# Kernel tuning notes

Hardware: AMD Instinct MI355X
Metric: run time of the kernel (lower is better)

Reference implementation:

```python
import jax, jax.numpy as jnp
import numpy as np

B_, L_, H_, P_ = 8, 4096, 512, 256
DT_LO, DT_HI = 1e-3, 4e-3  # keep Heinsen log-space weights in fp32 range for L=4096


def setup_inputs() -> dict:
    key = jax.random.key(0)
    ks = jax.random.split(key, 8)
    u = jax.random.normal(ks[0], (B_, L_, H_), dtype=jnp.float32)
    # Diagonal continuous-time state matrix Lambda (HiPPO-N-like: Re=-0.5, structured imag parts)
    lambda_re = -0.5 * jnp.ones((P_,), dtype=jnp.float32)
    lambda_im = jnp.pi * (jnp.arange(P_, dtype=jnp.float32) + 1.0)
    # Input/output projections (complex, stored as re/im pairs)
    B_re = jax.random.normal(ks[1], (P_, H_), dtype=jnp.float32) / jnp.sqrt(float(H_))
    B_im = jax.random.normal(ks[2], (P_, H_), dtype=jnp.float32) / jnp.sqrt(float(H_))
    C_re = jax.random.normal(ks[3], (H_, P_), dtype=jnp.float32) / jnp.sqrt(float(P_))
    C_im = jax.random.normal(ks[4], (H_, P_), dtype=jnp.float32) / jnp.sqrt(float(P_))
    D = jax.random.normal(ks[5], (H_,), dtype=jnp.float32)
    # Per-state learnable log-timescales, log-uniform in [DT_LO, DT_HI]
    log_delta = jax.random.uniform(ks[6], (P_,), dtype=jnp.float32,
                                   minval=jnp.log(DT_LO), maxval=jnp.log(DT_HI))
    return {"u": u, "lambda_re": lambda_re, "lambda_im": lambda_im,
            "B_re": B_re, "B_im": B_im, "C_re": C_re, "C_im": C_im,
            "D": D, "log_delta": log_delta}


def reference(u, lambda_re, lambda_im, B_re, B_im, C_re, C_im, D, log_delta):
    # --- ZOH discretization (eq. 6 of S5 paper) ---
    lam = lambda_re + 1j * lambda_im                     # (P,) complex64
    delta = jnp.exp(log_delta)                           # (P,)
    lambda_bar = jnp.exp(lam * delta)                    # (P,) complex
    B_tilde = B_re + 1j * B_im                           # (P,H)
    B_bar = ((lambda_bar - 1.0) / lam)[:, None] * B_tilde  # (P,H)

    # --- input projection: Bu_k = B_bar @ u_k ---
    Bu = jnp.einsum('blh,ph->blp', u.astype(B_bar.dtype), B_bar)  # (B,L,P) complex

    # --- Heinsen log-space parallel scan: x_k = lambda_bar * x_{k-1} + Bu_k ---
    L = u.shape[1]
    log_lambda = jnp.log(lambda_bar)                     # (P,) complex
    k = jnp.arange(L, dtype=jnp.float32)
    weights = jnp.exp(k[:, None] * log_lambda[None, :])  # (L,P) complex
    xs = weights[None] * jnp.cumsum(Bu / weights[None], axis=1)  # (B,L,P)

    # --- output: y_k = 2*Re(C_tilde x_k) + D*u_k (conjugate symmetry) ---
    C_tilde = C_re + 1j * C_im                           # (H,P)
    y = 2.0 * jnp.real(jnp.einsum('blp,hp->blh', xs, C_tilde)) + D * u
    return y
```

## Files before the change

kernel.cpp:

```cpp
#include <hip/hip_runtime.h>
#include <hip/hip_bf16.h>
#include <math.h>

#define HH 512
#define PP 256
#define LSEQ 4096
#define BB 8
#define MTOT (BB*LSEQ)
#define N2P 512

typedef __attribute__((ext_vector_type(8))) short bf16x8;
typedef __attribute__((ext_vector_type(4))) float f32x4;
typedef __attribute__((ext_vector_type(8))) unsigned short u16x8;
typedef __attribute__((ext_vector_type(4))) unsigned short u16x4;

#define SWZ(row) (((((row) & 7) ^ (((row) >> 3) & 7)) << 4))

__device__ inline unsigned short f2b(float x) {
    return __builtin_bit_cast(unsigned short, __float2bfloat16(x));
}
__device__ inline float b2f(unsigned short h) {
    union { unsigned int u; float f; } v; v.u = ((unsigned int)h) << 16;
    return v.f;
}

#define GLOAD16(gp, lp) __builtin_amdgcn_global_load_lds( \
    (const __attribute__((address_space(1))) unsigned int*)(gp), \
    (__attribute__((address_space(3))) unsigned int*)(lp), 16, 0, 0)

__device__ inline size_t panel_off(int r, int k) {
    int nblk = r >> 7, rl = r & 127;
    int kblk = k >> 6, kl = k & 63;
    int c = kl >> 3, j = kl & 7;
    return (size_t)(nblk * 8 + kblk) * 16384 + rl * 128 + ((c * 16) ^ SWZ(rl)) + j * 2;
}

__global__ void prep_w1_k(const float* __restrict__ lre, const float* __restrict__ lim,
                          const float* __restrict__ logd,
                          const float* __restrict__ Bre, const float* __restrict__ Bim,
                          char* __restrict__ W1s, float2* __restrict__ lamb) {
    int idx = blockIdx.x * 256 + threadIdx.x;
    if (idx >= PP * HH) return;
    int p = idx >> 9;
    int h = idx & (HH - 1);
    float delta = expf(logd[p]);
    float lr = lre[p], li = lim[p];
    float er = expf(lr * delta);
    float th = li * delta;
    float lbr = er * cosf(th), lbi = er * sinf(th);
    if (h == 0) lamb[p] = make_float2(lbr, lbi);
    float a = lbr - 1.0f, b = lbi;
    float n2 = lr * lr + li * li;
    float gr = (a * lr + b * li) / n2;
    float gi = (b * lr - a * li) / n2;
    float br = Bre[idx], bi = Bim[idx];
    *(unsigned short*)(W1s + panel_off(p, h))      = f2b(gr * br - gi * bi);
    *(unsigned short*)(W1s + panel_off(PP + p, h)) = f2b(gr * bi + gi * br);
}

__global__ void prep_w2_k(const float* __restrict__ Cre, const float* __restrict__ Cim,
                          char* __restrict__ W2s) {
    int idx = blockIdx.x * 256 + threadIdx.x;
    if (idx >= HH * N2P) return;
    int h = idx >> 9;
    int k = idx & 511;
    float v = (k < PP) ? 2.0f * Cre[(size_t)h * PP + k]
                       : -2.0f * Cim[(size_t)h * PP + (k - PP)];
    *(unsigned short*)(W2s + panel_off(h, k)) = f2b(v);
}

#define TILE_COMPUTE(ABUF, BBUF) { \
    bf16x8 af[4][2], bfv[2][2]; \
    _Pragma("unroll") for (int f = 0; f < 4; ++f) { \
      int ar = wm + f * 16 + (lane & 15); \
      _Pragma("unroll") for (int kk = 0; kk < 2; ++kk) \
        af[f][kk] = *(const bf16x8*)((ABUF) + ar * 128 + ((kk * 64 + (lane >> 4) * 16) ^ SWZ(ar))); } \
    _Pragma("unroll") for (int g = 0; g < 2; ++g) { \
      int br = wn + g * 16 + (lane & 15); \
      _Pragma("unroll") for (int kk = 0; kk < 2; ++kk) \
        bfv[g][kk] = *(const bf16x8*)((BBUF) + br * 128 + ((kk * 64 + (lane >> 4) * 16) ^ SWZ(br))); } \
    _Pragma("unroll") for (int f = 0; f < 4; ++f) \
      _Pragma("unroll") for (int g = 0; g < 2; ++g) \
        _Pragma("unroll") for (int kk = 0; kk < 2; ++kk) \
          acc[f][g] = __builtin_amdgcn_mfma_f32_16x16x32_bf16(af[f][kk], bfv[g][kk], acc[f][g], 0, 0, 0); }

__global__ __launch_bounds__(512, 4) void gemm1_k(const float* __restrict__ u,
                                                  const char* __restrict__ W1s,
                                                  unsigned short* __restrict__ T1) {
    __shared__ char smem[65536];
    const int tid = threadIdx.x, wave = tid >> 6, lane = tid & 63;
    const int swz = (blockIdx.x & 7) * 128 + (blockIdx.x >> 3);
    const int m0 = (swz >> 2) * 128;
    const int nblk = swz & 3, n0 = nblk * 128;
    const int wm = (wave >> 2) * 64, wn = (wave & 3) * 32;
    const int arow = tid >> 2, acol = tid & 3;

    float4 av[4];
    f32x4 acc[4][2] = {};

#define G1_A_LOAD(K0) { \
    const float* src = &u[(size_t)(m0 + arow) * HH + (K0) + acol * 16]; \
    av[0] = *(const float4*)src;       av[1] = *(const float4*)(src + 4); \
    av[2] = *(const float4*)(src + 8); av[3] = *(const float4*)(src + 12); }

#define G1_A_WRITE(ABUF) { \
    bf16x8 p0, p1; \
    p0[0] = (short)f2b(av[0].x); p0[1] = (short)f2b(av[0].y); \
    p0[2] = (short)f2b(av[0].z); p0[3] = (short)f2b(av[0].w); \
    p0[4] = (short)f2b(av[1].x); p0[5] = (short)f2b(av[1].y); \
    p0[6] = (short)f2b(av[1].z); p0[7] = (short)f2b(av[1].w); \
    p1[0] = (short)f2b(av[2].x); p1[1] = (short)f2b(av[2].y); \
    p1[2] = (short)f2b(av[2].z); p1[3] = (short)f2b(av[2].w); \
    p1[4] = (short)f2b(av[3].x); p1[5] = (short)f2b(av[3].y); \
    p1[6] = (short)f2b(av[3].z); p1[7] = (short)f2b(av[3].w); \
    *(bf16x8*)((ABUF) + arow * 128 + ((acol * 32)      ^ SWZ(arow))) = p0; \
    *(bf16x8*)((ABUF) + arow * 128 + ((acol * 32 + 16) ^ SWZ(arow))) = p1; }

#define G1_B_GLOAD(K0, BBUF) { \
    const char* pan = W1s + (size_t)(nblk * 8 + ((K0) >> 6)) * 16384 + tid * 16; \
    GLOAD16(pan, (BBUF) + tid * 16); \
    GLOAD16(pan + 8192, (BBUF) + tid * 16 + 8192); }

    char* A0 = smem;          char* B0 = smem + 16384;
    char* A1 = smem + 32768;  char* B1 = smem + 49152;

    G1_B_GLOAD(0, B0); G1_A_LOAD(0); G1_A_WRITE(A0);
    asm volatile("s_waitcnt vmcnt(0)" ::: "memory");
    __syncthreads();

    for (int t = 0; t < 8; ++t) {
        char* Ac = (t & 1) ? A1 : A0; char* Bc = (t & 1) ? B1 : B0;
        char* An = (t & 1) ? A0 : A1; char* Bn = (t & 1) ? B0 : B1;
        if (t < 7) { G1_B_GLOAD((t + 1) * 64, Bn); G1_A_LOAD((t + 1) * 64); }
        TILE_COMPUTE(Ac, Bc);
        if (t < 7) { G1_A_WRITE(An); }
        asm volatile("s_waitcnt vmcnt(0)" ::: "memory");
        __syncthreads();
    }

    {
        char* ep = smem;
        #pragma unroll
        for (int f = 0; f < 4; ++f) {
            #pragma unroll
            for (int g = 0; g < 2; ++g) {
                int r = wn + g * 16 + (lane & 15);
                int mb = (wm + f * 16 + ((lane >> 4) << 2)) * 2;
                u16x4 pk;
                pk[0] = f2b(acc[f][g][0]); pk[1] = f2b(acc[f][g][1]);
                pk[2] = f2b(acc[f][g][2]); pk[3] = f2b(acc[f][g][3]);
                *(u16x4*)(ep + r * 256 + (mb ^ ((r & 7) << 4))) = pk;
            }
        }
        __syncthreads();
        #pragma unroll
        for (int it = 0; it < 4; ++it) {
            int r = it * 32 + (tid >> 4);
            int mc = tid & 15;
            u16x8 v = *(const u16x8*)(ep + r * 256 + ((mc * 16) ^ ((r & 7) << 4)));
            *(u16x8*)&T1[(size_t)(n0 + r) * MTOT + m0 + mc * 8] = v;
        }
    }
}

__global__ __launch_bounds__(512, 4) void gemm2_k(const unsigned short* __restrict__ Xs,
                                                  const char* __restrict__ W2s,
                                                  float* __restrict__ y,
                                                  const float* __restrict__ u,
                                                  const float* __restrict__ D) {
    __shared__ char smem[65536];
    const int tid = threadIdx.x, wave = tid >> 6, lane = tid & 63;
    const int swz = (blockIdx.x & 7) * 128 + (blockIdx.x >> 3);
    const int m0 = (swz >> 2) * 128;
    const int nblk = swz & 3, n0 = nblk * 128;
    const int wm = (wave >> 2) * 64, wn = (wave & 3) * 32;
    const int kr = tid >> 5;
    const int mc4 = tid & 31;

    u16x4 xv[4];
    f32x4 acc[4][2] = {};

#define G2_A_LOAD(K0) { \
    _Pragma("unroll") for (int kk = 0; kk < 4; ++kk) \
        xv[kk] = *(const u16x4*)&Xs[(size_t)((K0) + kr * 4 + kk) * MTOT + m0 + mc4 * 4]; }

#define G2_A_WRITE(ABUF) { \
    _Pragma("unroll") for (int j = 0; j < 4; ++j) { \
        int m = mc4 * 4 + j; \
        u16x4 o; o[0] = xv[0][j]; o[1] = xv[1][j]; o[2] = xv[2][j]; o[3] = xv[3][j]; \
        *(u16x4*)((ABUF) + m * 128 + ((kr * 8) ^ SWZ(m))) = o; } }

#define G2_B_GLOAD(K0, BBUF) { \
    const char* pan = W2s + (size_t)(nblk * 8 + ((K0) >> 6)) * 16384 + tid * 16; \
    GLOAD16(pan, (BBUF) + tid * 16); \
    GLOAD16(pan + 8192, (BBUF) + tid * 16 + 8192); }

    char* A0 = smem;          char* B0 = smem + 16384;
    char* A1 = smem + 32768;  char* B1 = smem + 49152;

    G2_B_GLOAD(0, B0); G2_A_LOAD(0); G2_A_WRITE(A0);
    asm volatile("s_waitcnt vmcnt(0)" ::: "memory");
    __syncthreads();

    for (int t = 0; t < 8; ++t) {
        char* Ac = (t & 1) ? A1 : A0; char* Bc = (t & 1) ? B1 : B0;
        char* An = (t & 1) ? A0 : A1; char* Bn = (t & 1) ? B0 : B1;
        if (t < 7) { G2_B_GLOAD((t + 1) * 64, Bn); G2_A_LOAD((t + 1) * 64); }
        TILE_COMPUTE(Ac, Bc);
        if (t < 7) { G2_A_WRITE(An); }
        asm volatile("s_waitcnt vmcnt(0)" ::: "memory");
        __syncthreads();
    }

    float* epi = (float*)smem;
    float* myepi = epi + wave * 2048;
    #pragma unroll
    for (int f = 0; f < 4; ++f) {
        #pragma unroll
        for (int g = 0; g < 2; ++g) {
            int ml = f * 16 + ((lane >> 4) << 2);
            int hl = g * 16 + (lane & 15);
            #pragma unroll
            for (int i = 0; i < 4; ++i)
                myepi[(ml + i) * 32 + hl] = acc[f][g][i];
        }
    }
    __syncthreads();

    #pragma unroll
    for (int it = 0; it < 8; ++it) {
        int idx = it * 512 + tid;
        int ml = idx >> 5, c = idx & 31;
        int w = ((ml >> 6) << 2) + (c >> 3);
        const float4 v = *(const float4*)(epi + w * 2048 + (ml & 63) * 32 + (c & 7) * 4);
        int grow = m0 + ml, gcol = n0 + c * 4;
        const float4 uv = *(const float4*)&u[(size_t)grow * HH + gcol];
        const float4 dv = *(const float4*)&D[gcol];
        float4 o = make_float4(v.x + dv.x * uv.x, v.y + dv.y * uv.y,
                               v.z + dv.z * uv.z, v.w + dv.w * uv.w);
        *(float4*)&y[(size_t)grow * HH + gcol] = o;
    }
}

__global__ __launch_bounds__(256) void scan_k(const unsigned short* __restrict__ T1,
                                              unsigned short* __restrict__ Xs,
                                              const float2* __restrict__ lamb) {
    const int b = blockIdx.x >> 8;
    const int p = blockIdx.x & 255;
    const int t = threadIdx.x;
    const float2 L = lamb[p];

    const size_t baseRe = (size_t)p * MTOT + (size_t)b * LSEQ + t * 16;
    const size_t baseIm = (size_t)(PP + p) * MTOT + (size_t)b * LSEQ + t * 16;

    u16x8 r0 = *(const u16x8*)&T1[baseRe];
    u16x8 r1 = *(const u16x8*)&T1[baseRe + 8];
    u16x8 i0 = *(const u16x8*)&T1[baseIm];
    u16x8 i1 = *(const u16x8*)&T1[baseIm + 8];

    float re[16], im[16];
    #pragma unroll
    for (int j = 0; j < 8; ++j) {
        re[j] = b2f(r0[j]); re[8 + j] = b2f(r1[j]);
        im[j] = b2f(i0[j]); im[8 + j] = b2f(i1[j]);
    }

    float sr = 0.f, si = 0.f;
    #pragma unroll
    for (int j = 0; j < 16; ++j) {
        float nsr = L.x * sr - L.y * si + re[j];
        si = L.x * si + L.y * sr + im[j];
        sr = nsr;
    }

    __shared__ float cr[256], ci[256];
    cr[t] = sr; ci[t] = si;
    __syncthreads();

    float wr = L.x, wi = L.y;
    #pragma unroll
    for (int q = 0; q < 4; ++q) { float nr = wr * wr - wi * wi; wi = 2.f * wr * wi; wr = nr; }

    for (int off = 1; off < 256; off <<= 1) {
        float pr = 0.f, pi = 0.f;
        const bool has = (t >= off);
        if (has) { pr = cr[t - off]; pi = ci[t - off]; }
        __syncthreads();
        if (has) {
            sr += wr * pr - wi * pi;
            si += wr * pi + wi * pr;
            cr[t] = sr; ci[t] = si;
        }
        __syncthreads();
        float nr = wr * wr - wi * wi; wi = 2.f * wr * wi; wr = nr;
    }

    float xr = 0.f, xi = 0.f;
    if (t > 0) { xr = cr[t - 1]; xi = ci[t - 1]; }

    u16x8 o0, o1, o2, o3;
    #pragma unroll
    for (int j = 0; j < 16; ++j) {
        float nr = L.x * xr - L.y * xi + re[j];
        xi = L.x * xi + L.y * xr + im[j];
        xr = nr;
        if (j < 8) { o0[j] = f2b(xr); o2[j] = f2b(xi); }
        else       { o1[j - 8] = f2b(xr); o3[j - 8] = f2b(xi); }
    }
    *(u16x8*)&Xs[baseRe]     = o0;
    *(u16x8*)&Xs[baseRe + 8] = o1;
    *(u16x8*)&Xs[baseIm]     = o2;
    *(u16x8*)&Xs[baseIm + 8] = o3;
}


extern "C" void kernel_launch(void* const* d_in, const int* in_sizes, int n_in,
                              void* d_out, int out_size, void* d_ws, size_t ws_size,
                              hipStream_t stream) {
    const float* u    = (const float*)d_in[0];
    const float* lre  = (const float*)d_in[1];
    const float* lim  = (const float*)d_in[2];
    const float* Bre  = (const float*)d_in[3];
    const float* Bim  = (const float*)d_in[4];
    const float* Cre  = (const float*)d_in[5];
    const float* Cim  = (const float*)d_in[6];
    const float* Dv   = (const float*)d_in[7];
    const float* logd = (const float*)d_in[8];
    float* out = (float*)d_out;

    char* ws = (char*)d_ws;
    char*           W1s  = ws;
    char*           W2s  = ws + (512 << 10);
    float2*         lamb = (float2*)(ws + (1 << 20));
    unsigned short* Xs   = (unsigned short*)(ws + (1 << 20) + 4096);

    unsigned short* T1 = (unsigned short*)d_out;

    prep_w1_k<<<(PP * HH) / 256, 256, 0, stream>>>(lre, lim, logd, Bre, Bim, W1s, lamb);
    prep_w2_k<<<(HH * N2P) / 256, 256, 0, stream>>>(Cre, Cim, W2s);

    gemm1_k<<<1024, 512, 0, stream>>>(u, W1s, T1);
    scan_k<<<BB * PP, 256, 0, stream>>>(T1, Xs, lamb);
    gemm2_k<<<1024, 512, 0, stream>>>(Xs, W2s, out, u, Dv);
}
```

Measured before the change: 99.74 us.

## Prefetch A operand two K-tiles ahead with register double-buffering in both GEMMs

Both GEMM kernels now keep two register sets for the A-operand global loads and issue each load two iterations ahead. The per-iteration wait drops from a full vmcnt(0) to vmcnt(4), so loads for the following tile can stay in flight across the barrier. The goal is to hide global-load latency on the u and Xs streams behind MFMA compute. In exchange it uses more VGPRs, which may limit occupancy under the 512-thread launch bounds, and correctness now depends on hand-counted vmcnt values matching the order in which loads are issued.

```diff
diff --git a/kernel.cpp b/kernel.cpp
--- a/kernel.cpp
+++ b/kernel.cpp
@@ -95,24 +95,24 @@
     const int wm = (wave >> 2) * 64, wn = (wave & 3) * 32;
     const int arow = tid >> 2, acol = tid & 3;
 
-    float4 av[4];
+    float4 av0[4], av1[4];
     f32x4 acc[4][2] = {};
 
-#define G1_A_LOAD(K0) { \
+#define G1_A_LOAD(SET, K0) { \
     const float* src = &u[(size_t)(m0 + arow) * HH + (K0) + acol * 16]; \
-    av[0] = *(const float4*)src;       av[1] = *(const float4*)(src + 4); \
-    av[2] = *(const float4*)(src + 8); av[3] = *(const float4*)(src + 12); }
-
-#define G1_A_WRITE(ABUF) { \
+    SET[0] = *(const float4*)src;       SET[1] = *(const float4*)(src + 4); \
+    SET[2] = *(const float4*)(src + 8); SET[3] = *(const float4*)(src + 12); }
+
+#define G1_A_WRITE(SET, ABUF) { \
     bf16x8 p0, p1; \
-    p0[0] = (short)f2b(av[0].x); p0[1] = (short)f2b(av[0].y); \
-    p0[2] = (short)f2b(av[0].z); p0[3] = (short)f2b(av[0].w); \
-    p0[4] = (short)f2b(av[1].x); p0[5] = (short)f2b(av[1].y); \
-    p0[6] = (short)f2b(av[1].z); p0[7] = (short)f2b(av[1].w); \
-    p1[0] = (short)f2b(av[2].x); p1[1] = (short)f2b(av[2].y); \
-    p1[2] = (short)f2b(av[2].z); p1[3] = (short)f2b(av[2].w); \
-    p1[4] = (short)f2b(av[3].x); p1[5] = (short)f2b(av[3].y); \
-    p1[6] = (short)f2b(av[3].z); p1[7] = (short)f2b(av[3].w); \
+    p0[0] = (short)f2b(SET[0].x); p0[1] = (short)f2b(SET[0].y); \
+    p0[2] = (short)f2b(SET[0].z); p0[3] = (short)f2b(SET[0].w); \
+    p0[4] = (short)f2b(SET[1].x); p0[5] = (short)f2b(SET[1].y); \
+    p0[6] = (short)f2b(SET[1].z); p0[7] = (short)f2b(SET[1].w); \
+    p1[0] = (short)f2b(SET[2].x); p1[1] = (short)f2b(SET[2].y); \
+    p1[2] = (short)f2b(SET[2].z); p1[3] = (short)f2b(SET[2].w); \
+    p1[4] = (short)f2b(SET[3].x); p1[5] = (short)f2b(SET[3].y); \
+    p1[6] = (short)f2b(SET[3].z); p1[7] = (short)f2b(SET[3].w); \
     *(bf16x8*)((ABUF) + arow * 128 + ((acol * 32)      ^ SWZ(arow))) = p0; \
     *(bf16x8*)((ABUF) + arow * 128 + ((acol * 32 + 16) ^ SWZ(arow))) = p1; }
 
@@ -124,17 +124,29 @@
     char* A0 = smem;          char* B0 = smem + 16384;
     char* A1 = smem + 32768;  char* B1 = smem + 49152;
 
-    G1_B_GLOAD(0, B0); G1_A_LOAD(0); G1_A_WRITE(A0);
-    asm volatile("s_waitcnt vmcnt(0)" ::: "memory");
+    G1_A_LOAD(av1, 0);
+    G1_B_GLOAD(0, B0);
+    G1_A_LOAD(av0, 64);
+    asm volatile("s_waitcnt vmcnt(4)" ::: "memory");
+    G1_A_WRITE(av1, A0);
     __syncthreads();
 
+    #pragma unroll
     for (int t = 0; t < 8; ++t) {
         char* Ac = (t & 1) ? A1 : A0; char* Bc = (t & 1) ? B1 : B0;
         char* An = (t & 1) ? A0 : A1; char* Bn = (t & 1) ? B0 : B1;
-        if (t < 7) { G1_B_GLOAD((t + 1) * 64, Bn); G1_A_LOAD((t + 1) * 64); }
+        if (t < 7) G1_B_GLOAD((t + 1) * 64, Bn);
+        if (t < 6) {
+            if ((t & 1) == 0) { G1_A_LOAD(av1, (t + 2) * 64); }
+            else              { G1_A_LOAD(av0, (t + 2) * 64); }
+        }
         TILE_COMPUTE(Ac, Bc);
-        if (t < 7) { G1_A_WRITE(An); }
-        asm volatile("s_waitcnt vmcnt(0)" ::: "memory");
+        if (t < 7) {
+            if ((t & 1) == 0) { G1_A_WRITE(av0, An); }
+            else              { G1_A_WRITE(av1, An); }
+        }
+        if (t < 6)       { asm volatile("s_waitcnt vmcnt(4)" ::: "memory"); }
+        else if (t == 6) { asm volatile("s_waitcnt vmcnt(0)" ::: "memory"); }
         __syncthreads();
     }
 
@@ -177,17 +189,17 @@
     const int kr = tid >> 5;
     const int mc4 = tid & 31;
 
-    u16x4 xv[4];
+    u16x4 xv0[4], xv1[4];
     f32x4 acc[4][2] = {};
 
-#define G2_A_LOAD(K0) { \
+#define G2_A_LOAD(SET, K0) { \
     _Pragma("unroll") for (int kk = 0; kk < 4; ++kk) \
-        xv[kk] = *(const u16x4*)&Xs[(size_t)((K0) + kr * 4 + kk) * MTOT + m0 + mc4 * 4]; }
-
-#define G2_A_WRITE(ABUF) { \
+        SET[kk] = *(const u16x4*)&Xs[(size_t)((K0) + kr * 4 + kk) * MTOT + m0 + mc4 * 4]; }
+
+#define G2_A_WRITE(SET, ABUF) { \
     _Pragma("unroll") for (int j = 0; j < 4; ++j) { \
         int m = mc4 * 4 + j; \
-        u16x4 o; o[0] = xv[0][j]; o[1] = xv[1][j]; o[2] = xv[2][j]; o[3] = xv[3][j]; \
+        u16x4 o; o[0] = SET[0][j]; o[1] = SET[1][j]; o[2] = SET[2][j]; o[3] = SET[3][j]; \
         *(u16x4*)((ABUF) + m * 128 + ((kr * 8) ^ SWZ(m))) = o; } }
 
 #define G2_B_GLOAD(K0, BBUF) { \
@@ -198,17 +210,29 @@
     char* A0 = smem;          char* B0 = smem + 16384;
     char* A1 = smem + 32768;  char* B1 = smem + 49152;
 
-    G2_B_GLOAD(0, B0); G2_A_LOAD(0); G2_A_WRITE(A0);
-    asm volatile("s_waitcnt vmcnt(0)" ::: "memory");
+    G2_A_LOAD(xv1, 0);
+    G2_B_GLOAD(0, B0);
+    G2_A_LOAD(xv0, 64);
+    asm volatile("s_waitcnt vmcnt(4)" ::: "memory");
+    G2_A_WRITE(xv1, A0);
     __syncthreads();
 
+    #pragma unroll
     for (int t = 0; t < 8; ++t) {
         char* Ac = (t & 1) ? A1 : A0; char* Bc = (t & 1) ? B1 : B0;
         char* An = (t & 1) ? A0 : A1; char* Bn = (t & 1) ? B0 : B1;
-        if (t < 7) { G2_B_GLOAD((t + 1) * 64, Bn); G2_A_LOAD((t + 1) * 64); }
+        if (t < 7) G2_B_GLOAD((t + 1) * 64, Bn);
+        if (t < 6) {
+            if ((t & 1) == 0) { G2_A_LOAD(xv1, (t + 2) * 64); }
+            else              { G2_A_LOAD(xv0, (t + 2) * 64); }
+        }
         TILE_COMPUTE(Ac, Bc);
-        if (t < 7) { G2_A_WRITE(An); }
-        asm volatile("s_waitcnt vmcnt(0)" ::: "memory");
+        if (t < 7) {
+            if ((t & 1) == 0) { G2_A_WRITE(xv0, An); }
+            else              { G2_A_WRITE(xv1, An); }
+        }
+        if (t < 6)       { asm volatile("s_waitcnt vmcnt(4)" ::: "memory"); }
+        else if (t == 6) { asm volatile("s_waitcnt vmcnt(0)" ::: "memory"); }
         __syncthreads();
     }
 
```

Result: faster. 97.48 us, median of 2 (-2.3%).

## Enlarge GEMM block tiles to 256x256 with larger per-wave register tiles

Applied to the files above, without the earlier changes.

Both GEMM kernels move from 128x128 block tiles to 256x256, each wave computing a 128x64 tile with 8x4 MFMA accumulators. The grid shrinks from 1024 to 256 blocks and LDS use doubles to 128KB. MFMA bursts are wrapped in s_setprio and followed by a sched_barrier, and the gemm2 epilogue is redone in two halves to fit LDS. The aim is more operand reuse and less global and LDS traffic per FLOP. The cost is higher register pressure, lower occupancy, and only 256 blocks, which may leave compute units underused.

```diff
diff --git a/kernel.cpp b/kernel.cpp
--- a/kernel.cpp
+++ b/kernel.cpp
@@ -70,69 +70,70 @@
 }
 
 #define TILE_COMPUTE(ABUF, BBUF) { \
-    bf16x8 af[4][2], bfv[2][2]; \
-    _Pragma("unroll") for (int f = 0; f < 4; ++f) { \
-      int ar = wm + f * 16 + (lane & 15); \
-      _Pragma("unroll") for (int kk = 0; kk < 2; ++kk) \
-        af[f][kk] = *(const bf16x8*)((ABUF) + ar * 128 + ((kk * 64 + (lane >> 4) * 16) ^ SWZ(ar))); } \
-    _Pragma("unroll") for (int g = 0; g < 2; ++g) { \
-      int br = wn + g * 16 + (lane & 15); \
-      _Pragma("unroll") for (int kk = 0; kk < 2; ++kk) \
-        bfv[g][kk] = *(const bf16x8*)((BBUF) + br * 128 + ((kk * 64 + (lane >> 4) * 16) ^ SWZ(br))); } \
-    _Pragma("unroll") for (int f = 0; f < 4; ++f) \
-      _Pragma("unroll") for (int g = 0; g < 2; ++g) \
-        _Pragma("unroll") for (int kk = 0; kk < 2; ++kk) \
-          acc[f][g] = __builtin_amdgcn_mfma_f32_16x16x32_bf16(af[f][kk], bfv[g][kk], acc[f][g], 0, 0, 0); }
-
-__global__ __launch_bounds__(512, 4) void gemm1_k(const float* __restrict__ u,
+    _Pragma("unroll") for (int kk = 0; kk < 2; ++kk) { \
+        bf16x8 af[8], bfv[4]; \
+        _Pragma("unroll") for (int f = 0; f < 8; ++f) { \
+            int ar = wm + f * 16 + (lane & 15); \
+            af[f] = *(const bf16x8*)((ABUF) + ar * 128 + ((kk * 64 + (lane >> 4) * 16) ^ SWZ(ar))); } \
+        _Pragma("unroll") for (int g = 0; g < 4; ++g) { \
+            int br = wn + g * 16 + (lane & 15); \
+            bfv[g] = *(const bf16x8*)((BBUF) + br * 128 + ((kk * 64 + (lane >> 4) * 16) ^ SWZ(br))); } \
+        __builtin_amdgcn_s_setprio(1); \
+        _Pragma("unroll") for (int f = 0; f < 8; ++f) \
+            _Pragma("unroll") for (int g = 0; g < 4; ++g) \
+                acc[f][g] = __builtin_amdgcn_mfma_f32_16x16x32_bf16(af[f], bfv[g], acc[f][g], 0, 0, 0); \
+        __builtin_amdgcn_s_setprio(0); } }
+
+#define B_GLOAD(WS, NB2, K0, BBUF) { \
+    const char* _p0 = (WS) + (size_t)((NB2) * 8 + ((K0) >> 6)) * 16384 + tid * 16; \
+    const char* _p1 = (WS) + (size_t)(((NB2) + 1) * 8 + ((K0) >> 6)) * 16384 + tid * 16; \
+    GLOAD16(_p0, (BBUF) + tid * 16); \
+    GLOAD16(_p0 + 8192, (BBUF) + tid * 16 + 8192); \
+    GLOAD16(_p1, (BBUF) + tid * 16 + 16384); \
+    GLOAD16(_p1 + 8192, (BBUF) + tid * 16 + 24576); }
+
+__global__ __launch_bounds__(512, 2) void gemm1_k(const float* __restrict__ u,
                                                   const char* __restrict__ W1s,
                                                   unsigned short* __restrict__ T1) {
-    __shared__ char smem[65536];
+    __shared__ char smem[131072];
     const int tid = threadIdx.x, wave = tid >> 6, lane = tid & 63;
-    const int swz = (blockIdx.x & 7) * 128 + (blockIdx.x >> 3);
-    const int m0 = (swz >> 2) * 128;
-    const int nblk = swz & 3, n0 = nblk * 128;
-    const int wm = (wave >> 2) * 64, wn = (wave & 3) * 32;
-    const int arow = tid >> 2, acol = tid & 3;
-
-    float4 av[4];
-    f32x4 acc[4][2] = {};
+    const int swz = (blockIdx.x & 7) * 32 + (blockIdx.x >> 3);
+    const int m0 = (swz >> 1) * 256;
+    const int nb2 = (swz & 1) * 2;
+    const int n0 = (swz & 1) * 256;
+    const int wm = (wave >> 2) * 128, wn = (wave & 3) * 64;
+    const int arow = tid >> 1, ahalf = tid & 1;
+
+    float4 av[8];
+    f32x4 acc[8][4] = {};
 
 #define G1_A_LOAD(K0) { \
-    const float* src = &u[(size_t)(m0 + arow) * HH + (K0) + acol * 16]; \
-    av[0] = *(const float4*)src;       av[1] = *(const float4*)(src + 4); \
-    av[2] = *(const float4*)(src + 8); av[3] = *(const float4*)(src + 12); }
+    const float* src = &u[(size_t)(m0 + arow) * HH + (K0) + ahalf * 32]; \
+    _Pragma("unroll") for (int q = 0; q < 8; ++q) av[q] = *(const float4*)(src + q * 4); }
 
 #define G1_A_WRITE(ABUF) { \
-    bf16x8 p0, p1; \
-    p0[0] = (short)f2b(av[0].x); p0[1] = (short)f2b(av[0].y); \
-    p0[2] = (short)f2b(av[0].z); p0[3] = (short)f2b(av[0].w); \
-    p0[4] = (short)f2b(av[1].x); p0[5] = (short)f2b(av[1].y); \
-    p0[6] = (short)f2b(av[1].z); p0[7] = (short)f2b(av[1].w); \
-    p1[0] = (short)f2b(av[2].x); p1[1] = (short)f2b(av[2].y); \
-    p1[2] = (short)f2b(av[2].z); p1[3] = (short)f2b(av[2].w); \
-    p1[4] = (short)f2b(av[3].x); p1[5] = (short)f2b(av[3].y); \
-    p1[6] = (short)f2b(av[3].z); p1[7] = (short)f2b(av[3].w); \
-    *(bf16x8*)((ABUF) + arow * 128 + ((acol * 32)      ^ SWZ(arow))) = p0; \
-    *(bf16x8*)((ABUF) + arow * 128 + ((acol * 32 + 16) ^ SWZ(arow))) = p1; }
-
-#define G1_B_GLOAD(K0, BBUF) { \
-    const char* pan = W1s + (size_t)(nblk * 8 + ((K0) >> 6)) * 16384 + tid * 16; \
-    GLOAD16(pan, (BBUF) + tid * 16); \
-    GLOAD16(pan + 8192, (BBUF) + tid * 16 + 8192); }
-
-    char* A0 = smem;          char* B0 = smem + 16384;
-    char* A1 = smem + 32768;  char* B1 = smem + 49152;
-
-    G1_B_GLOAD(0, B0); G1_A_LOAD(0); G1_A_WRITE(A0);
+    _Pragma("unroll") for (int c = 0; c < 4; ++c) { \
+        bf16x8 pk; \
+        pk[0] = (short)f2b(av[2*c].x); pk[1] = (short)f2b(av[2*c].y); \
+        pk[2] = (short)f2b(av[2*c].z); pk[3] = (short)f2b(av[2*c].w); \
+        pk[4] = (short)f2b(av[2*c+1].x); pk[5] = (short)f2b(av[2*c+1].y); \
+        pk[6] = (short)f2b(av[2*c+1].z); pk[7] = (short)f2b(av[2*c+1].w); \
+        *(bf16x8*)((ABUF) + arow * 128 + ((ahalf * 64 + c * 16) ^ SWZ(arow))) = pk; } }
+
+    char* A0 = smem;          char* A1 = smem + 32768;
+    char* B0 = smem + 65536;  char* B1 = smem + 98304;
+
+    G1_A_LOAD(0); B_GLOAD(W1s, nb2, 0, B0); G1_A_WRITE(A0);
     asm volatile("s_waitcnt vmcnt(0)" ::: "memory");
     __syncthreads();
 
+    #pragma unroll
     for (int t = 0; t < 8; ++t) {
         char* Ac = (t & 1) ? A1 : A0; char* Bc = (t & 1) ? B1 : B0;
         char* An = (t & 1) ? A0 : A1; char* Bn = (t & 1) ? B0 : B1;
-        if (t < 7) { G1_B_GLOAD((t + 1) * 64, Bn); G1_A_LOAD((t + 1) * 64); }
+        if (t < 7) { B_GLOAD(W1s, nb2, (t + 1) * 64, Bn); G1_A_LOAD((t + 1) * 64); }
         TILE_COMPUTE(Ac, Bc);
+        __builtin_amdgcn_sched_barrier(0);
         if (t < 7) { G1_A_WRITE(An); }
         asm volatile("s_waitcnt vmcnt(0)" ::: "memory");
         __syncthreads();
@@ -141,104 +142,107 @@
     {
         char* ep = smem;
         #pragma unroll
-        for (int f = 0; f < 4; ++f) {
+        for (int f = 0; f < 8; ++f) {
             #pragma unroll
-            for (int g = 0; g < 2; ++g) {
+            for (int g = 0; g < 4; ++g) {
                 int r = wn + g * 16 + (lane & 15);
                 int mb = (wm + f * 16 + ((lane >> 4) << 2)) * 2;
                 u16x4 pk;
                 pk[0] = f2b(acc[f][g][0]); pk[1] = f2b(acc[f][g][1]);
                 pk[2] = f2b(acc[f][g][2]); pk[3] = f2b(acc[f][g][3]);
-                *(u16x4*)(ep + r * 256 + (mb ^ ((r & 7) << 4))) = pk;
+                *(u16x4*)(ep + r * 512 + (mb ^ SWZ(r))) = pk;
             }
         }
         __syncthreads();
         #pragma unroll
-        for (int it = 0; it < 4; ++it) {
-            int r = it * 32 + (tid >> 4);
-            int mc = tid & 15;
-            u16x8 v = *(const u16x8*)(ep + r * 256 + ((mc * 16) ^ ((r & 7) << 4)));
+        for (int it = 0; it < 16; ++it) {
+            int idx = it * 512 + tid;
+            int r = idx >> 5, mc = idx & 31;
+            u16x8 v = *(const u16x8*)(ep + r * 512 + ((mc * 16) ^ SWZ(r)));
             *(u16x8*)&T1[(size_t)(n0 + r) * MTOT + m0 + mc * 8] = v;
         }
     }
 }
 
-__global__ __launch_bounds__(512, 4) void gemm2_k(const unsigned short* __restrict__ Xs,
+__global__ __launch_bounds__(512, 2) void gemm2_k(const unsigned short* __restrict__ Xs,
                                                   const char* __restrict__ W2s,
                                                   float* __restrict__ y,
                                                   const float* __restrict__ u,
                                                   const float* __restrict__ D) {
-    __shared__ char smem[65536];
+    __shared__ char smem[131072];
     const int tid = threadIdx.x, wave = tid >> 6, lane = tid & 63;
-    const int swz = (blockIdx.x & 7) * 128 + (blockIdx.x >> 3);
-    const int m0 = (swz >> 2) * 128;
-    const int nblk = swz & 3, n0 = nblk * 128;
-    const int wm = (wave >> 2) * 64, wn = (wave & 3) * 32;
+    const int swz = (blockIdx.x & 7) * 32 + (blockIdx.x >> 3);
+    const int m0 = (swz >> 1) * 256;
+    const int nb2 = (swz & 1) * 2;
+    const int n0 = (swz & 1) * 256;
+    const int wm = (wave >> 2) * 128, wn = (wave & 3) * 64;
     const int kr = tid >> 5;
-    const int mc4 = tid & 31;
-
-    u16x4 xv[4];
-    f32x4 acc[4][2] = {};
+    const int mc8 = tid & 31;
+
+    u16x8 xv[4];
+    f32x4 acc[8][4] = {};
 
 #define G2_A_LOAD(K0) { \
     _Pragma("unroll") for (int kk = 0; kk < 4; ++kk) \
-        xv[kk] = *(const u16x4*)&Xs[(size_t)((K0) + kr * 4 + kk) * MTOT + m0 + mc4 * 4]; }
+        xv[kk] = *(const u16x8*)&Xs[(size_t)((K0) + kr * 4 + kk) * MTOT + m0 + mc8 * 8]; }
 
 #define G2_A_WRITE(ABUF) { \
-    _Pragma("unroll") for (int j = 0; j < 4; ++j) { \
-        int m = mc4 * 4 + j; \
+    _Pragma("unroll") for (int j = 0; j < 8; ++j) { \
+        int m = mc8 * 8 + j; \
         u16x4 o; o[0] = xv[0][j]; o[1] = xv[1][j]; o[2] = xv[2][j]; o[3] = xv[3][j]; \
         *(u16x4*)((ABUF) + m * 128 + ((kr * 8) ^ SWZ(m))) = o; } }
 
-#define G2_B_GLOAD(K0, BBUF) { \
-    const char* pan = W2s + (size_t)(nblk * 8 + ((K0) >> 6)) * 16384 + tid * 16; \
-    GLOAD16(pan, (BBUF) + tid * 16); \
-    GLOAD16(pan + 8192, (BBUF) + tid * 16 + 8192); }
-
-    char* A0 = smem;          char* B0 = smem + 16384;
-    char* A1 = smem + 32768;  char* B1 = smem + 49152;
-
-    G2_B_GLOAD(0, B0); G2_A_LOAD(0); G2_A_WRITE(A0);
+    char* A0 = smem;          char* A1 = smem + 32768;
+    char* B0 = smem + 65536;  char* B1 = smem + 98304;
+
+    G2_A_LOAD(0); B_GLOAD(W2s, nb2, 0, B0); G2_A_WRITE(A0);
     asm volatile("s_waitcnt vmcnt(0)" ::: "memory");
     __syncthreads();
 
+    #pragma unroll
     for (int t = 0; t < 8; ++t) {
         char* Ac = (t & 1) ? A1 : A0; char* Bc = (t & 1) ? B1 : B0;
         char* An = (t & 1) ? A0 : A1; char* Bn = (t & 1) ? B0 : B1;
-        if (t < 7) { G2_B_GLOAD((t + 1) * 64, Bn); G2_A_LOAD((t + 1) * 64); }
+        if (t < 7) { B_GLOAD(W2s, nb2, (t + 1) * 64, Bn); G2_A_LOAD((t + 1) * 64); }
         TILE_COMPUTE(Ac, Bc);
+        __builtin_amdgcn_sched_barrier(0);
         if (t < 7) { G2_A_WRITE(An); }
         asm volatile("s_waitcnt vmcnt(0)" ::: "memory");
         __syncthreads();
     }
 
-    float* epi = (float*)smem;
-    float* myepi = epi + wave * 2048;
-    #pragma unroll
-    for (int f = 0; f < 4; ++f) {
+    float* ep = (float*)smem;
+    #pragma unroll
+    for (int half = 0; half < 2; ++half) {
+        if ((wave >> 2) == half) {
+            #pragma unroll
+            for (int f = 0; f < 8; ++f) {
+                #pragma unroll
+                for (int g = 0; g < 4; ++g) {
+                    int ml = f * 16 + ((lane >> 4) << 2);
+                    int hl = wn + g * 16 + (lane & 15);
+                    #pragma unroll
+                    for (int i = 0; i < 4; ++i) {
+                        int mr = ml + i;
+                        ep[mr * 256 + (hl ^ ((mr & 7) << 2))] = acc[f][g][i];
+                    }
+                }
+            }
+        }
+        __syncthreads();
         #pragma unroll
-        for (int g = 0; g < 2; ++g) {
-            int ml = f * 16 + ((lane >> 4) << 2);
-            int hl = g * 16 + (lane & 15);
-            #pragma unroll
-            for (int i = 0; i < 4; ++i)
-                myepi[(ml + i) * 32 + hl] = acc[f][g][i];
-        }
-    }
-    __syncthreads();
-
-    #pragma unroll
-    for (int it = 0; it < 8; ++it) {
-        int idx = it * 512 + tid;
-        int ml = idx >> 5, c = idx & 31;
-        int w = ((ml >> 6) << 2) + (c >> 3);
-        const float4 v = *(const float4*)(epi + w * 2048 + (ml & 63) * 32 + (c & 7) * 4);
-        int grow = m0 + ml, gcol = n0 + c * 4;
-        const float4 uv = *(const float4*)&u[(size_t)grow * HH + gcol];
-        const float4 dv = *(const float4*)&D[gcol];
-        float4 o = make_float4(v.x + dv.x * uv.x, v.y + dv.y * uv.y,
-                               v.z + dv.z * uv.z, v.w + dv.w * uv.w);
-        *(float4*)&y[(size_t)grow * HH + gcol] = o;
+        for (int it = 0; it < 16; ++it) {
+            int idx = it * 512 + tid;
+            int ml = idx >> 6, c = idx & 63;
+            const f32x4 v = *(const f32x4*)&ep[ml * 256 + ((c * 4) ^ ((ml & 7) << 2))];
+            int mg = m0 + half * 128 + ml, hg = n0 + c * 4;
+            const float4 uv = *(const float4*)&u[(size_t)mg * HH + hg];
+            const float4 dv = *(const float4*)&D[hg];
+            float4 o = make_float4(v[0] + dv.x * uv.x, v[1] + dv.y * uv.y,
+                                   v[2] + dv.z * uv.z, v[3] + dv.w * uv.w);
+            *(float4*)&y[(size_t)mg * HH + hg] = o;
+        }
+        __syncthreads();
     }
 }
 
@@ -339,7 +343,7 @@
     prep_w1_k<<<(PP * HH) / 256, 256, 0, stream>>>(lre, lim, logd, Bre, Bim, W1s, lamb);
     prep_w2_k<<<(HH * N2P) / 256, 256, 0, stream>>>(Cre, Cim, W2s);
 
-    gemm1_k<<<1024, 512, 0, stream>>>(u, W1s, T1);
+    gemm1_k<<<256, 512, 0, stream>>>(u, W1s, T1);
     scan_k<<<BB * PP, 256, 0, stream>>>(T1, Xs, lamb);
-    gemm2_k<<<1024, 512, 0, stream>>>(Xs, W2s, out, u, Dv);
-}
+    gemm2_k<<<256, 512, 0, stream>>>(Xs, W2s, out, u, Dv);
+}
```

Measured after the change: 98.46 us. No clear change (-1.3%).
